# Optimization experiments

Hardware: AMD Instinct MI355X
Metric: run time of the kernel (lower is better)

## Reference

```python
import jax, jax.numpy as jnp
import numpy as np

B, L, H, K = 16, 65536, 64, 64


def setup_inputs() -> dict:
    key = jax.random.key(0)
    k1, k2 = jax.random.split(key, 2)
    x = jax.random.normal(k1, (B, L), dtype=jnp.float32)
    W = jax.random.normal(k2, (K, H), dtype=jnp.float32) * 0.02  # nn.Linear weight [K, H]
    b = jnp.zeros((K,), dtype=jnp.float32)
    return {"x": x, "W": W, "b": b}


def reference(x, W, b):
    # x: [B, L]; W: [K, H]; b: [K]
    Hh = W.shape[1]
    Bb, Ll = x.shape
    xpad = jnp.pad(x, ((0, 0), (Hh - 1, 0)))  # left-pad like F.pad(x, (H-1, 0))
    # Hankel windows: windows[b, t, j] = xpad[b, t + j]  -> [B, L, H]
    idx = jnp.arange(Ll)[:, None] + jnp.arange(Hh)[None, :]
    windows = xpad[:, idx]
    mu = windows.mean(axis=2, keepdims=True)
    sd = windows.std(axis=2, keepdims=True, ddof=1)  # torch std is unbiased (ddof=1)
    wn = (windows - mu) / (sd + 1e-6)
    d2 = jax.nn.relu(jnp.einsum('blh,kh->blk', wn, W) + b)
    warmup = Hh - 1
    return (d2[:, warmup:, :], warmup)
```

## Files before the change

### kernel.cpp

```cpp
#include <hip/hip_runtime.h>
#include <hip/hip_bf16.h>
#include <stdint.h>

#define LCOUNT 65536
#define LOUT   65473
#define KF     64
#define HH     64
#define TL     1024
#define ROW    1096

typedef __attribute__((ext_vector_type(8))) short  short8;
typedef __attribute__((ext_vector_type(4))) float  float4v;
typedef __attribute__((ext_vector_type(2))) float  float2v;

__device__ __forceinline__ unsigned short f2bf(float f) {
    union { float f; uint32_t u; } c; c.f = f;
    uint32_t u = c.u;
    u += 0x7FFFu + ((u >> 16) & 1u);
    return (unsigned short)(u >> 16);
}

__global__ __launch_bounds__(256, 4)
void hankel_kernel(const float* __restrict__ x,
                   const float* __restrict__ W,
                   const float* __restrict__ bias,
                   float* __restrict__ out)
{
    __shared__ __align__(16) float          xs_f[TL + 64];
    __shared__ __align__(16) unsigned short rep[8 * ROW];
    __shared__ __align__(16) float          muinv_s[2 * TL];
    __shared__ float wsum_s[KF];
    __shared__ float bias_s[KF];

    const int tid  = threadIdx.x;
    const int lane = tid & 63;
    const int wv   = tid >> 6;
    const int m    = lane & 15;
    const int quad = lane >> 4;

    const int tile     = blockIdx.x;
    const int bb       = blockIdx.y;
    const int block_lo = tile * TL;

    {
        const float4v* xrow4 = (const float4v*)(x + (size_t)bb * LCOUNT);
        const int base4 = block_lo >> 2;
        const int nf4   = (TL + 64) / 4;
        for (int i4 = tid; i4 < nf4; i4 += 256) {
            int g4 = base4 + i4;
            if (g4 > LCOUNT / 4 - 1) g4 = LCOUNT / 4 - 1;
            float4v v = xrow4[g4];
            *(float4v*)(xs_f + 4 * i4) = v;
            uint32_t plo = (uint32_t)f2bf(v[0]) | ((uint32_t)f2bf(v[1]) << 16);
            uint32_t phi = (uint32_t)f2bf(v[2]) | ((uint32_t)f2bf(v[3]) << 16);
            *(uint2*)(rep + 4 * i4) = make_uint2(plo, phi);
        }
    }

    if (tid < KF) {
        const float4v* wr = (const float4v*)(W + tid * HH);
        float s = 0.f;
        #pragma unroll
        for (int i = 0; i < HH / 4; ++i) {
            float4v w = wr[i];
            s += w[0] + w[1] + w[2] + w[3];
        }
        wsum_s[tid] = s;
        bias_s[tid] = bias[tid];
    }

    short8 afrag[4][2];
    #pragma unroll
    for (int t = 0; t < 4; ++t) {
        const int k = t * 16 + m;
        #pragma unroll
        for (int ki = 0; ki < 2; ++ki) {
            const float4v* wp = (const float4v*)(W + k * HH + quad * 8 + ki * 32);
            float4v w0 = wp[0];
            float4v w1 = wp[1];
            short8 f;
            f[0] = (short)f2bf(w0[0]); f[1] = (short)f2bf(w0[1]);
            f[2] = (short)f2bf(w0[2]); f[3] = (short)f2bf(w0[3]);
            f[4] = (short)f2bf(w1[0]); f[5] = (short)f2bf(w1[1]);
            f[6] = (short)f2bf(w1[2]); f[7] = (short)f2bf(w1[3]);
            afrag[t][ki] = f;
        }
    }

    __syncthreads();

    {
        const int p0 = 4 * tid;
        const float4v* xv = (const float4v*)(xs_f + p0);
        float s1 = 0.f, s2 = 0.f;
        float4v v0 = xv[0];
        float4v v16 = xv[16];
        #pragma unroll
        for (int i = 0; i < 16; ++i) {
            float4v v = xv[i];
            s1 += v[0] + v[1] + v[2] + v[3];
            s2 += v[0] * v[0] + v[1] * v[1] + v[2] * v[2] + v[3] * v[3];
        }
        float mu4[4], inv4[4];
        #pragma unroll
        for (int i = 0; i < 4; ++i) {
            if (i > 0) {
                float xo = v0[i - 1], xn = v16[i - 1];
                s1 += xn - xo;
                s2 += xn * xn - xo * xo;
            }
            float mu  = s1 * (1.f / 64.f);
            float var = (s2 - 64.f * mu * mu) * (1.f / 63.f);
            var = var < 0.f ? 0.f : var;
            mu4[i]  = mu;
            inv4[i] = 1.f / (sqrtf(var) + 1e-6f);
        }
        float4v lo4, hi4;
        lo4[0] = mu4[0]; lo4[1] = inv4[0]; lo4[2] = mu4[1]; lo4[3] = inv4[1];
        hi4[0] = mu4[2]; hi4[1] = inv4[2]; hi4[2] = mu4[3]; hi4[3] = inv4[3];
        *(float4v*)(muinv_s + 8 * tid)     = lo4;
        *(float4v*)(muinv_s + 8 * tid + 4) = hi4;
    }

    for (int tt = tid; tt < 1080; tt += 256) {
        const int s = tt & 7;
        const int c = tt >> 3;
        if (s) {
            const int i0 = 8 * c + s;
            short8 w;
            #pragma unroll
            for (int j = 0; j < 8; ++j) w[j] = (short)rep[i0 + j];
            *(short8*)(rep + s * ROW + 8 * c) = w;
        }
    }
    __syncthreads();

    const unsigned short* myrow = rep + (m & 7) * ROW + (m & 8) + quad * 8;

    for (int g = wv; g < TL / 16; g += 4) {
        const int p0 = g * 16;

        short8 b0 = *(const short8*)(myrow + p0);
        short8 b1 = *(const short8*)(myrow + p0 + 32);

        float2v mi = *(const float2v*)(muinv_s + 2 * (p0 + m));
        const float muv  = mi[0];
        const float invv = mi[1];
        const int   lo   = block_lo + p0 + m;

        float4v acc[4];
        #pragma unroll
        for (int t = 0; t < 4; ++t) acc[t] = (float4v){0.f, 0.f, 0.f, 0.f};

        #pragma unroll
        for (int t = 0; t < 4; ++t) {
            acc[t] = __builtin_amdgcn_mfma_f32_16x16x32_bf16(afrag[t][0], b0, acc[t], 0, 0, 0);
            acc[t] = __builtin_amdgcn_mfma_f32_16x16x32_bf16(afrag[t][1], b1, acc[t], 0, 0, 0);
        }

        if (lo < LOUT) {
            float* op = out + ((size_t)bb * LOUT + lo) * KF + quad * 4;
            #pragma unroll
            for (int t = 0; t < 4; ++t) {
                float4v ws = *(const float4v*)(wsum_s + t * 16 + quad * 4);
                float4v bs = *(const float4v*)(bias_s + t * 16 + quad * 4);
                float4v v;
                #pragma unroll
                for (int r = 0; r < 4; ++r) {
                    float vv = (acc[t][r] - muv * ws[r]) * invv + bs[r];
                    v[r] = vv > 0.f ? vv : 0.f;
                }
                *(float4v*)(op + t * 16) = v;
            }
        }
    }

    if (tile == 0 && bb == 0 && tid == 0) {
        out[(size_t)16 * LOUT * KF] = 63.0f;
    }
}

extern "C" void kernel_launch(void* const* d_in, const int* in_sizes, int n_in,
                              void* d_out, int out_size, void* d_ws, size_t ws_size,
                              hipStream_t stream) {
    const float* x = (const float*)d_in[0];
    const float* W = (const float*)d_in[1];
    const float* b = (const float*)d_in[2];
    float* out = (float*)d_out;

    dim3 grid((LOUT + TL - 1) / TL, 16);
    hankel_kernel<<<grid, 256, 0, stream>>>(x, W, b, out);
}
```

Baseline: 279.7 us.

## Stage MFMA outputs through per-wave LDS bounce buffer for contiguous row stores

```diff
diff --git a/kernel.cpp b/kernel.cpp
--- a/kernel.cpp
+++ b/kernel.cpp
@@ -7,9 +7,11 @@
 #define KF     64
 #define HH     64
 #define TL     1024
-#define ROW    1096
+#define ROW4   1104
+#define BSTR   68
 
 typedef __attribute__((ext_vector_type(8))) short  short8;
+typedef __attribute__((ext_vector_type(4))) short  short4v;
 typedef __attribute__((ext_vector_type(4))) float  float4v;
 typedef __attribute__((ext_vector_type(2))) float  float2v;
 
@@ -27,10 +29,11 @@
                    float* __restrict__ out)
 {
     __shared__ __align__(16) float          xs_f[TL + 64];
-    __shared__ __align__(16) unsigned short rep[8 * ROW];
+    __shared__ __align__(16) unsigned short rep4[4 * ROW4];
     __shared__ __align__(16) float          muinv_s[2 * TL];
     __shared__ float wsum_s[KF];
     __shared__ float bias_s[KF];
+    __shared__ __align__(16) float          bounce[4][16 * BSTR];
 
     const int tid  = threadIdx.x;
     const int lane = tid & 63;
@@ -53,7 +56,7 @@
             *(float4v*)(xs_f + 4 * i4) = v;
             uint32_t plo = (uint32_t)f2bf(v[0]) | ((uint32_t)f2bf(v[1]) << 16);
             uint32_t phi = (uint32_t)f2bf(v[2]) | ((uint32_t)f2bf(v[3]) << 16);
-            *(uint2*)(rep + 4 * i4) = make_uint2(plo, phi);
+            *(uint2*)(rep4 + 4 * i4) = make_uint2(plo, phi);
         }
     }
 
@@ -122,31 +125,38 @@
         *(float4v*)(muinv_s + 8 * tid + 4) = hi4;
     }
 
-    for (int tt = tid; tt < 1080; tt += 256) {
-        const int s = tt & 7;
-        const int c = tt >> 3;
+    for (int tt = tid; tt < 544; tt += 256) {
+        const int s = tt & 3;
+        const int c = tt >> 2;
         if (s) {
             const int i0 = 8 * c + s;
             short8 w;
             #pragma unroll
-            for (int j = 0; j < 8; ++j) w[j] = (short)rep[i0 + j];
-            *(short8*)(rep + s * ROW + 8 * c) = w;
+            for (int j = 0; j < 8; ++j) w[j] = (short)rep4[i0 + j];
+            *(short8*)(rep4 + s * ROW4 + 8 * c) = w;
         }
     }
     __syncthreads();
 
-    const unsigned short* myrow = rep + (m & 7) * ROW + (m & 8) + quad * 8;
+    const unsigned short* myrow = rep4 + (m & 3) * ROW4 + (m & 12) + quad * 8;
+    float* const bw   = &bounce[wv][0];
+    float* const outb = out + (size_t)bb * LOUT * KF;
+    const int kh     = 4 * (lane & 15);
+    const int prow   = lane >> 4;
 
     for (int g = wv; g < TL / 16; g += 4) {
         const int p0 = g * 16;
 
-        short8 b0 = *(const short8*)(myrow + p0);
-        short8 b1 = *(const short8*)(myrow + p0 + 32);
+        short4v a0 = *(const short4v*)(myrow + p0);
+        short4v a1 = *(const short4v*)(myrow + p0 + 4);
+        short4v a2 = *(const short4v*)(myrow + p0 + 32);
+        short4v a3 = *(const short4v*)(myrow + p0 + 36);
+        short8 b0 = __builtin_shufflevector(a0, a1, 0, 1, 2, 3, 4, 5, 6, 7);
+        short8 b1 = __builtin_shufflevector(a2, a3, 0, 1, 2, 3, 4, 5, 6, 7);
 
         float2v mi = *(const float2v*)(muinv_s + 2 * (p0 + m));
-        const float muv  = mi[0];
         const float invv = mi[1];
-        const int   lo   = block_lo + p0 + m;
+        const float nmi  = -mi[0] * invv;
 
         float4v acc[4];
         #pragma unroll
@@ -158,21 +168,29 @@
             acc[t] = __builtin_amdgcn_mfma_f32_16x16x32_bf16(afrag[t][1], b1, acc[t], 0, 0, 0);
         }
 
-        if (lo < LOUT) {
-            float* op = out + ((size_t)bb * LOUT + lo) * KF + quad * 4;
+        #pragma unroll
+        for (int t = 0; t < 4; ++t) {
+            float4v ws = *(const float4v*)(wsum_s + t * 16 + quad * 4);
+            float4v bs = *(const float4v*)(bias_s + t * 16 + quad * 4);
+            float4v v;
             #pragma unroll
-            for (int t = 0; t < 4; ++t) {
-                float4v ws = *(const float4v*)(wsum_s + t * 16 + quad * 4);
-                float4v bs = *(const float4v*)(bias_s + t * 16 + quad * 4);
-                float4v v;
-                #pragma unroll
-                for (int r = 0; r < 4; ++r) {
-                    float vv = (acc[t][r] - muv * ws[r]) * invv + bs[r];
-                    v[r] = vv > 0.f ? vv : 0.f;
-                }
-                *(float4v*)(op + t * 16) = v;
+            for (int r = 0; r < 4; ++r) {
+                float vv = fmaf(acc[t][r], invv, fmaf(nmi, ws[r], bs[r]));
+                v[r] = vv > 0.f ? vv : 0.f;
             }
-        }
+            *(float4v*)(bw + m * BSTR + t * 16 + quad * 4) = v;
+        }
+        asm volatile("s_waitcnt lgkmcnt(0)" ::: "memory");
+        #pragma unroll
+        for (int s = 0; s < 4; ++s) {
+            const int pos_in = 4 * s + prow;
+            float4v v = *(const float4v*)(bw + pos_in * BSTR + kh);
+            const int pos = block_lo + p0 + pos_in;
+            if (pos < LOUT) {
+                *(float4v*)(outb + (size_t)pos * KF + kh) = v;
+            }
+        }
+        asm volatile("" ::: "memory");
     }
 
     if (tile == 0 && bb == 0 && tid == 0) {
```

After: 274.3 us. Within noise of the previous version (-1.9%).
